# Kernel tuning notes

Measured on AMD Instinct MI355X. Metric: run time of the kernel, lower is better.

## Reference

```python
import jax, jax.numpy as jnp
import numpy as np

B, N, D, H = 2, 2048, 1024, 16
DH = D // H
SCALE = DH ** -0.5

def setup_inputs() -> dict:
    key = jax.random.key(0)
    k1, k2, k3 = jax.random.split(key, 3)
    x = jax.random.normal(k1, (B, N, D), dtype=jnp.float32)
    W_qkv = jax.random.normal(k2, (3 * D, D), dtype=jnp.float32) * (D ** -0.5)
    W_out = jax.random.normal(k3, (D, D), dtype=jnp.float32) * (D ** -0.5)
    mask = jnp.tril(jnp.ones((N, N), dtype=jnp.int32))  # causal mask; 0 -> -inf
    return {"x": x, "mask": mask, "W_qkv": W_qkv, "W_out": W_out}

def reference(x, mask, W_qkv, W_out):
    b, n, d = x.shape
    qkv = x @ W_qkv.T                                   # [B,N,3D]
    qkv = qkv.reshape(b, n, 3, H, DH).transpose(2, 0, 3, 1, 4)  # [3,B,H,N,DH]
    q, k, v = qkv[0], qkv[1], qkv[2]
    attn = jnp.einsum('bhqd,bhkd->bhqk', q, k) * SCALE  # [B,H,N,N]
    attn = jnp.where(mask == 0, -jnp.inf, attn)
    attn = jax.nn.softmax(attn, axis=-1)
    out = jnp.einsum('bhqk,bhkd->bhqd', attn, v)        # [B,H,N,DH]
    out = out.transpose(0, 2, 1, 3).reshape(b, n, d)    # [B,N,D]
    return out @ W_out.T
```

## Files before the change

### kernel.cpp

```cpp
#include <hip/hip_runtime.h>
#include <hip/hip_bf16.h>


typedef __hip_bfloat16 bf16;
typedef short bf16x8 __attribute__((ext_vector_type(8)));
typedef short bf16x4 __attribute__((ext_vector_type(4)));
typedef float f32x4 __attribute__((ext_vector_type(4)));

#define QSCALE 0.1803368801111204f

__device__ __forceinline__ short f2bf(float f) {
    __hip_bfloat16 h = __float2bfloat16(f);
    return *reinterpret_cast<short*>(&h);
}

__device__ __forceinline__ unsigned pack_bf16(float a, float b) {
    unsigned au = __builtin_bit_cast(unsigned, a) + 0x8000u;
    unsigned bu = __builtin_bit_cast(unsigned, b) + 0x8000u;
    return __builtin_amdgcn_perm(bu, au, 0x07060302u);
}

__global__ void cast4(const float* __restrict__ src, bf16* __restrict__ dst, int n4) {
    int i = blockIdx.x * blockDim.x + threadIdx.x;
    if (i < n4) {
        float4 f = reinterpret_cast<const float4*>(src)[i];
        short4 s;
        s.x = f2bf(f.x); s.y = f2bf(f.y); s.z = f2bf(f.z); s.w = f2bf(f.w);
        reinterpret_cast<short4*>(dst)[i] = s;
    }
}

template<int EPI>
__global__ __launch_bounds__(256)
void gemm_bt(const bf16* __restrict__ A, const bf16* __restrict__ Bt,
             float* __restrict__ Cf,
             bf16* __restrict__ qp, bf16* __restrict__ kp, bf16* __restrict__ vp,
             int K, int Ncols) {
    __shared__ alignas(16) short As[64][40];
    __shared__ alignas(16) short Bs[64][40];
    const int tid = threadIdx.x;
    const int wave = tid >> 6, lane = tid & 63;
    const int quad = lane >> 4, l16 = lane & 15;
    const int m0 = blockIdx.x * 64;
    const int n0 = blockIdx.y * 64;

    f32x4 acc[4] = {};

    const int sr = tid >> 2;
    const int sc = (tid & 3) * 8;
    const bf16* Aptr = A + (size_t)(m0 + sr) * K + sc;
    const bf16* Bptr = Bt + (size_t)(n0 + sr) * K + sc;

    for (int k0 = 0; k0 < K; k0 += 32) {
        bf16x8 av = *reinterpret_cast<const bf16x8*>(Aptr + k0);
        bf16x8 bv = *reinterpret_cast<const bf16x8*>(Bptr + k0);
        __syncthreads();
        *reinterpret_cast<bf16x8*>(&As[sr][sc]) = av;
        *reinterpret_cast<bf16x8*>(&Bs[sr][sc]) = bv;
        __syncthreads();
        bf16x8 af = *reinterpret_cast<const bf16x8*>(&As[wave * 16 + l16][quad * 8]);
        #pragma unroll
        for (int nt = 0; nt < 4; ++nt) {
            bf16x8 bfr = *reinterpret_cast<const bf16x8*>(&Bs[nt * 16 + l16][quad * 8]);
            acc[nt] = __builtin_amdgcn_mfma_f32_16x16x32_bf16(af, bfr, acc[nt], 0, 0, 0);
        }
    }

    #pragma unroll
    for (int nt = 0; nt < 4; ++nt) {
        #pragma unroll
        for (int r = 0; r < 4; ++r) {
            int gm = m0 + wave * 16 + quad * 4 + r;
            int gn = n0 + nt * 16 + l16;
            float val = acc[nt][r];
            if (EPI == 0) {
                int sel = gn >> 10, rem = gn & 1023;
                int h = rem >> 6, dh = rem & 63;
                int b = gm >> 11, nq = gm & 2047;
                if (sel == 0) val *= QSCALE;
                bf16* dst = (sel == 0) ? qp : ((sel == 1) ? kp : vp);
                dst[((((size_t)b * 16 + h) * 2048) + nq) * 64 + dh] = __float2bfloat16(val);
            } else {
                Cf[(size_t)gm * Ncols + gn] = val;
            }
        }
    }
}

__global__ __launch_bounds__(256)
void flash_attn(const bf16* __restrict__ Q, const bf16* __restrict__ K,
                const bf16* __restrict__ V, bf16* __restrict__ O) {
    __shared__ alignas(16) short Ks[2][64][72];
    __shared__ alignas(16) short Vt[2][64][68];

    const int tid = threadIdx.x;
    const int wave = tid >> 6, lane = tid & 63;
    const int quad = lane >> 4, l16 = lane & 15;
    const int bh = blockIdx.x;
    const int yy = blockIdx.y;
    const int g = yy & 7, kq = yy >> 3;
    const int qt = (kq == 0) ? g : (kq == 1) ? (15 - g) : (kq == 2) ? (16 + g) : (31 - g);
    const int q0 = qt * 64;
    const float NEG_INF = -__builtin_inff();

    const bf16* Qb = Q + (size_t)bh * 2048 * 64;
    const bf16* Kb = K + (size_t)bh * 2048 * 64;
    const bf16* Vb = V + (size_t)bh * 2048 * 64;

    const int qrow = q0 + wave * 16 + l16;
    const bf16x8 qf0 = *reinterpret_cast<const bf16x8*>(Qb + (size_t)qrow * 64 + quad * 8);
    const bf16x8 qf1 = *reinterpret_cast<const bf16x8*>(Qb + (size_t)qrow * 64 + 32 + quad * 8);

    float l_part = 0.f;
    f32x4 o[4] = {};

    const int krow = tid >> 2;
    const int kcol = (tid & 3) * 16;
    const int kb = (tid & 15) * 4;
    const int db = (tid >> 4) * 4;

    {
        bf16x8 a0 = *reinterpret_cast<const bf16x8*>(Kb + (size_t)krow * 64 + kcol);
        bf16x8 a1 = *reinterpret_cast<const bf16x8*>(Kb + (size_t)krow * 64 + kcol + 8);
        bf16x4 L0 = *reinterpret_cast<const bf16x4*>(Vb + (size_t)(kb + 0) * 64 + db);
        bf16x4 L1 = *reinterpret_cast<const bf16x4*>(Vb + (size_t)(kb + 1) * 64 + db);
        bf16x4 L2 = *reinterpret_cast<const bf16x4*>(Vb + (size_t)(kb + 2) * 64 + db);
        bf16x4 L3 = *reinterpret_cast<const bf16x4*>(Vb + (size_t)(kb + 3) * 64 + db);
        *reinterpret_cast<bf16x8*>(&Ks[0][krow][kcol]) = a0;
        *reinterpret_cast<bf16x8*>(&Ks[0][krow][kcol + 8]) = a1;
        #pragma unroll
        for (int j = 0; j < 4; ++j) {
            bf16x4 w; w[0] = L0[j]; w[1] = L1[j]; w[2] = L2[j]; w[3] = L3[j];
            *reinterpret_cast<bf16x4*>(&Vt[0][db + j][kb]) = w;
        }
    }
    __syncthreads();

    int buf = 0;
    for (int j0 = 0; j0 < q0; j0 += 64) {
        const bf16* Kn = Kb + (size_t)(j0 + 64) * 64;
        const bf16* Vn = Vb + (size_t)(j0 + 64) * 64;
        bf16x8 nk0 = *reinterpret_cast<const bf16x8*>(Kn + (size_t)krow * 64 + kcol);
        bf16x8 nk1 = *reinterpret_cast<const bf16x8*>(Kn + (size_t)krow * 64 + kcol + 8);
        bf16x4 N0 = *reinterpret_cast<const bf16x4*>(Vn + (size_t)(kb + 0) * 64 + db);
        bf16x4 N1 = *reinterpret_cast<const bf16x4*>(Vn + (size_t)(kb + 1) * 64 + db);
        bf16x4 N2 = *reinterpret_cast<const bf16x4*>(Vn + (size_t)(kb + 2) * 64 + db);
        bf16x4 N3 = *reinterpret_cast<const bf16x4*>(Vn + (size_t)(kb + 3) * 64 + db);

        f32x4 s[4];
        #pragma unroll
        for (int t = 0; t < 4; ++t) {
            bf16x8 k0 = *reinterpret_cast<const bf16x8*>(&Ks[buf][16 * t + l16][quad * 8]);
            bf16x8 k1 = *reinterpret_cast<const bf16x8*>(&Ks[buf][16 * t + l16][32 + quad * 8]);
            f32x4 a = {};
            a = __builtin_amdgcn_mfma_f32_16x16x32_bf16(k0, qf0, a, 0, 0, 0);
            a = __builtin_amdgcn_mfma_f32_16x16x32_bf16(k1, qf1, a, 0, 0, 0);
            s[t] = a;
        }

        bf16x4 pk[4];
        #pragma unroll
        for (int t = 0; t < 4; ++t) {
            float p0 = __builtin_amdgcn_exp2f(s[t][0]);
            float p1 = __builtin_amdgcn_exp2f(s[t][1]);
            float p2 = __builtin_amdgcn_exp2f(s[t][2]);
            float p3 = __builtin_amdgcn_exp2f(s[t][3]);
            l_part += (p0 + p1) + (p2 + p3);
            unsigned* pku = reinterpret_cast<unsigned*>(&pk[t]);
            pku[0] = pack_bf16(p0, p1);
            pku[1] = pack_bf16(p2, p3);
        }

        #pragma unroll
        for (int t = 0; t < 4; ++t) {
            #pragma unroll
            for (int dt = 0; dt < 4; ++dt) {
                bf16x4 vf = *reinterpret_cast<const bf16x4*>(
                    &Vt[buf][dt * 16 + l16][t * 16 + quad * 4]);
                o[dt] = __builtin_amdgcn_mfma_f32_16x16x16bf16_1k(vf, pk[t], o[dt], 0, 0, 0);
            }
        }

        *reinterpret_cast<bf16x8*>(&Ks[buf ^ 1][krow][kcol]) = nk0;
        *reinterpret_cast<bf16x8*>(&Ks[buf ^ 1][krow][kcol + 8]) = nk1;
        #pragma unroll
        for (int j = 0; j < 4; ++j) {
            bf16x4 w; w[0] = N0[j]; w[1] = N1[j]; w[2] = N2[j]; w[3] = N3[j];
            *reinterpret_cast<bf16x4*>(&Vt[buf ^ 1][db + j][kb]) = w;
        }
        __syncthreads();
        buf ^= 1;
    }

    {
        f32x4 s[4];
        #pragma unroll
        for (int t = 0; t < 4; ++t) {
            if (t <= wave) {
                bf16x8 k0 = *reinterpret_cast<const bf16x8*>(&Ks[buf][16 * t + l16][quad * 8]);
                bf16x8 k1 = *reinterpret_cast<const bf16x8*>(&Ks[buf][16 * t + l16][32 + quad * 8]);
                f32x4 a = {};
                a = __builtin_amdgcn_mfma_f32_16x16x32_bf16(k0, qf0, a, 0, 0, 0);
                a = __builtin_amdgcn_mfma_f32_16x16x32_bf16(k1, qf1, a, 0, 0, 0);
                if (t == wave) {
                    #pragma unroll
                    for (int r = 0; r < 4; ++r)
                        if (quad * 4 + r > l16) a[r] = NEG_INF;
                }
                s[t] = a;
            }
        }
        bf16x4 pk[4];
        #pragma unroll
        for (int t = 0; t < 4; ++t) {
            if (t <= wave) {
                float p0 = __builtin_amdgcn_exp2f(s[t][0]);
                float p1 = __builtin_amdgcn_exp2f(s[t][1]);
                float p2 = __builtin_amdgcn_exp2f(s[t][2]);
                float p3 = __builtin_amdgcn_exp2f(s[t][3]);
                l_part += (p0 + p1) + (p2 + p3);
                unsigned* pku = reinterpret_cast<unsigned*>(&pk[t]);
                pku[0] = pack_bf16(p0, p1);
                pku[1] = pack_bf16(p2, p3);
            }
        }
        #pragma unroll
        for (int t = 0; t < 4; ++t) {
            if (t <= wave) {
                #pragma unroll
                for (int dt = 0; dt < 4; ++dt) {
                    bf16x4 vf = *reinterpret_cast<const bf16x4*>(
                        &Vt[buf][dt * 16 + l16][t * 16 + quad * 4]);
                    o[dt] = __builtin_amdgcn_mfma_f32_16x16x16bf16_1k(vf, pk[t], o[dt], 0, 0, 0);
                }
            }
        }
    }

    float l = l_part;
    l += __shfl_xor(l, 16, 64);
    l += __shfl_xor(l, 32, 64);
    const float inv = 1.f / l;

    const int b = bh >> 4, h = bh & 15;
    bf16* orow = O + ((size_t)b * 2048 + qrow) * 1024 + h * 64;
    #pragma unroll
    for (int dt = 0; dt < 4; ++dt) {
        bf16x4 w;
        unsigned* wu = reinterpret_cast<unsigned*>(&w);
        wu[0] = pack_bf16(o[dt][0] * inv, o[dt][1] * inv);
        wu[1] = pack_bf16(o[dt][2] * inv, o[dt][3] * inv);
        *reinterpret_cast<bf16x4*>(orow + dt * 16 + quad * 4) = w;
    }
}

extern "C" void kernel_launch(void* const* d_in, const int* in_sizes, int n_in,
                              void* d_out, int out_size, void* d_ws, size_t ws_size,
                              hipStream_t stream) {
    const float* x    = (const float*)d_in[0];
    const float* Wqkv = (const float*)d_in[2];
    const float* Wout = (const float*)d_in[3];
    float* out = (float*)d_out;

    char* ws = (char*)d_ws;
    bf16* x_bf    = (bf16*)(ws);
    bf16* wqkv_bf = (bf16*)(ws + 8388608);
    bf16* wout_bf = (bf16*)(ws + 14680064);
    bf16* q       = (bf16*)(ws + 16777216);
    bf16* k       = (bf16*)(ws + 25165824);
    bf16* v       = (bf16*)(ws + 33554432);
    bf16* ao      = (bf16*)(ws + 41943040);

    cast4<<<4096, 256, 0, stream>>>(x, x_bf, 1048576);
    cast4<<<3072, 256, 0, stream>>>(Wqkv, wqkv_bf, 786432);
    cast4<<<1024, 256, 0, stream>>>(Wout, wout_bf, 262144);

    gemm_bt<0><<<dim3(64, 48), 256, 0, stream>>>(x_bf, wqkv_bf, nullptr, q, k, v, 1024, 3072);
    flash_attn<<<dim3(32, 32), 256, 0, stream>>>(q, k, v, ao);
    gemm_bt<1><<<dim3(64, 16), 256, 0, stream>>>(ao, wout_bf, out, nullptr, nullptr, nullptr, 1024, 1024);
}
```

Baseline: 214.8 us.

## Rewrite GEMMs with 128x128 tiles, async global-to-LDS loads and double buffering

Both projection GEMMs move from 64x64 tiles with one wave per 16-row strip to 128x128 tiles where each wave computes a 64x64 sub-block (16 MFMAs per k-step). Operand tiles are loaded straight into LDS with global_load_lds, using XOR-swizzled columns to avoid bank conflicts. They are double-buffered so the next k-slice's loads overlap the current MFMAs, with one barrier per iteration instead of two. This raises arithmetic intensity and cuts global traffic and sync overhead. The cost is more register pressure and fewer blocks: 768 and 256 instead of 3072 and 1024, which may underfill 256 CUs for the output GEMM.

```diff
diff --git a/kernel.cpp b/kernel.cpp
--- a/kernel.cpp
+++ b/kernel.cpp
@@ -8,6 +8,13 @@
 typedef float f32x4 __attribute__((ext_vector_type(4)));
 
 #define QSCALE 0.1803368801111204f
+
+typedef __attribute__((address_space(3))) unsigned int lds_u32;
+typedef const __attribute__((address_space(1))) unsigned int glob_u32;
+
+__device__ __forceinline__ void glds16(const void* g, void* l) {
+    __builtin_amdgcn_global_load_lds((glob_u32*)g, (lds_u32*)l, 16, 0, 0);
+}
 
 __device__ __forceinline__ short f2bf(float f) {
     __hip_bfloat16 h = __float2bfloat16(f);
@@ -32,56 +39,91 @@
 
 template<int EPI>
 __global__ __launch_bounds__(256)
-void gemm_bt(const bf16* __restrict__ A, const bf16* __restrict__ Bt,
+void gemm128(const bf16* __restrict__ A, const bf16* __restrict__ Bt,
              float* __restrict__ Cf,
              bf16* __restrict__ qp, bf16* __restrict__ kp, bf16* __restrict__ vp,
              int K, int Ncols) {
-    __shared__ alignas(16) short As[64][40];
-    __shared__ alignas(16) short Bs[64][40];
+    __shared__ alignas(16) short As[2][4096];
+    __shared__ alignas(16) short Bs[2][4096];
+
     const int tid = threadIdx.x;
     const int wave = tid >> 6, lane = tid & 63;
     const int quad = lane >> 4, l16 = lane & 15;
-    const int m0 = blockIdx.x * 64;
-    const int n0 = blockIdx.y * 64;
-
-    f32x4 acc[4] = {};
-
-    const int sr = tid >> 2;
-    const int sc = (tid & 3) * 8;
-    const bf16* Aptr = A + (size_t)(m0 + sr) * K + sc;
-    const bf16* Bptr = Bt + (size_t)(n0 + sr) * K + sc;
-
-    for (int k0 = 0; k0 < K; k0 += 32) {
-        bf16x8 av = *reinterpret_cast<const bf16x8*>(Aptr + k0);
-        bf16x8 bv = *reinterpret_cast<const bf16x8*>(Bptr + k0);
+    const int wm = wave >> 1, wn = wave & 1;
+    const int m0 = blockIdx.x * 128;
+    const int n0 = blockIdx.y * 128;
+
+    f32x4 acc[4][4] = {};
+
+    const int srow = tid >> 2;
+    const int skk  = (((tid & 3) ^ ((tid >> 3) & 3))) * 8;
+    const bf16* Ag = A  + (size_t)(m0 + srow) * K + skk;
+    const bf16* Bg = Bt + (size_t)(n0 + srow) * K + skk;
+    const size_t rowskip = (size_t)64 * K;
+    short* Asl = &As[0][0] + tid * 8;
+    short* Bsl = &Bs[0][0] + tid * 8;
+
+    const int xk = (quad ^ ((l16 >> 1) & 3)) * 8;
+    const int arow = wm * 64 + l16;
+    const int brow = wn * 64 + l16;
+
+    const int KI = K >> 5;
+    glds16(Ag, Asl);
+    glds16(Ag + rowskip, Asl + 2048);
+    glds16(Bg, Bsl);
+    glds16(Bg + rowskip, Bsl + 2048);
+    __syncthreads();
+
+    int buf = 0;
+    for (int ki = 0; ki < KI; ++ki) {
+        if (ki + 1 < KI) {
+            const bf16* ag = Ag + (ki + 1) * 32;
+            const bf16* bg = Bg + (ki + 1) * 32;
+            short* ad = Asl + (buf ^ 1) * 4096;
+            short* bd = Bsl + (buf ^ 1) * 4096;
+            glds16(ag, ad);
+            glds16(ag + rowskip, ad + 2048);
+            glds16(bg, bd);
+            glds16(bg + rowskip, bd + 2048);
+        }
+        const short* ab = &As[buf][0];
+        const short* bb = &Bs[buf][0];
+        bf16x8 af[4], bf[4];
+        #pragma unroll
+        for (int mt = 0; mt < 4; ++mt)
+            af[mt] = *reinterpret_cast<const bf16x8*>(ab + (arow + mt * 16) * 32 + xk);
+        #pragma unroll
+        for (int nt = 0; nt < 4; ++nt)
+            bf[nt] = *reinterpret_cast<const bf16x8*>(bb + (brow + nt * 16) * 32 + xk);
+        #pragma unroll
+        for (int mt = 0; mt < 4; ++mt)
+            #pragma unroll
+            for (int nt = 0; nt < 4; ++nt)
+                acc[mt][nt] = __builtin_amdgcn_mfma_f32_16x16x32_bf16(
+                    af[mt], bf[nt], acc[mt][nt], 0, 0, 0);
         __syncthreads();
-        *reinterpret_cast<bf16x8*>(&As[sr][sc]) = av;
-        *reinterpret_cast<bf16x8*>(&Bs[sr][sc]) = bv;
-        __syncthreads();
-        bf16x8 af = *reinterpret_cast<const bf16x8*>(&As[wave * 16 + l16][quad * 8]);
+        buf ^= 1;
+    }
+
+    #pragma unroll
+    for (int mt = 0; mt < 4; ++mt) {
         #pragma unroll
         for (int nt = 0; nt < 4; ++nt) {
-            bf16x8 bfr = *reinterpret_cast<const bf16x8*>(&Bs[nt * 16 + l16][quad * 8]);
-            acc[nt] = __builtin_amdgcn_mfma_f32_16x16x32_bf16(af, bfr, acc[nt], 0, 0, 0);
-        }
-    }
-
-    #pragma unroll
-    for (int nt = 0; nt < 4; ++nt) {
-        #pragma unroll
-        for (int r = 0; r < 4; ++r) {
-            int gm = m0 + wave * 16 + quad * 4 + r;
-            int gn = n0 + nt * 16 + l16;
-            float val = acc[nt][r];
-            if (EPI == 0) {
-                int sel = gn >> 10, rem = gn & 1023;
-                int h = rem >> 6, dh = rem & 63;
-                int b = gm >> 11, nq = gm & 2047;
-                if (sel == 0) val *= QSCALE;
-                bf16* dst = (sel == 0) ? qp : ((sel == 1) ? kp : vp);
-                dst[((((size_t)b * 16 + h) * 2048) + nq) * 64 + dh] = __float2bfloat16(val);
-            } else {
-                Cf[(size_t)gm * Ncols + gn] = val;
+            #pragma unroll
+            for (int r = 0; r < 4; ++r) {
+                int gm = m0 + wm * 64 + mt * 16 + quad * 4 + r;
+                int gn = n0 + wn * 64 + nt * 16 + l16;
+                float val = acc[mt][nt][r];
+                if (EPI == 0) {
+                    int sel = gn >> 10, rem = gn & 1023;
+                    int h = rem >> 6, dh = rem & 63;
+                    int b = gm >> 11, nq = gm & 2047;
+                    if (sel == 0) val *= QSCALE;
+                    bf16* dst = (sel == 0) ? qp : ((sel == 1) ? kp : vp);
+                    dst[((((size_t)b * 16 + h) * 2048) + nq) * 64 + dh] = __float2bfloat16(val);
+                } else {
+                    Cf[(size_t)gm * Ncols + gn] = val;
+                }
             }
         }
     }
@@ -275,7 +317,7 @@
     cast4<<<3072, 256, 0, stream>>>(Wqkv, wqkv_bf, 786432);
     cast4<<<1024, 256, 0, stream>>>(Wout, wout_bf, 262144);
 
-    gemm_bt<0><<<dim3(64, 48), 256, 0, stream>>>(x_bf, wqkv_bf, nullptr, q, k, v, 1024, 3072);
+    gemm128<0><<<dim3(32, 24), 256, 0, stream>>>(x_bf, wqkv_bf, nullptr, q, k, v, 1024, 3072);
     flash_attn<<<dim3(32, 32), 256, 0, stream>>>(q, k, v, ao);
-    gemm_bt<1><<<dim3(64, 16), 256, 0, stream>>>(ao, wout_bf, out, nullptr, nullptr, nullptr, 1024, 1024);
-}
+    gemm128<1><<<dim3(32, 8), 256, 0, stream>>>(ao, wout_bf, out, nullptr, nullptr, nullptr, 1024, 1024);
+}
```

Measured after the change: 189.2 us. 1.14x faster.
